# Kernel optimization log

Hardware: AMD Instinct MI355X
Metric: run time of the kernel (lower is better)

Reference implementation:

```python
import jax, jax.numpy as jnp
import numpy as np
import math

H_DIM = 256
EPS = 1e-5


def _bn(x, g, b):
    # BatchNorm1d in training mode: batch stats, biased variance
    mu = x.mean(0)
    var = jnp.var(x, 0)
    return (x - mu) * jax.lax.rsqrt(var + EPS) * g + b


def _batched_corrcoef(x):
    # x: (B, s, n) -> (B, n, n) correlation over n variables with s samples
    xm = x - x.mean(1, keepdims=True)
    c = jnp.einsum('bsi,bsj->bij', xm, xm) / (x.shape[1] - 1)
    d = jnp.sqrt(jnp.diagonal(c, axis1=1, axis2=2))
    c = c / (d[:, :, None] * d[:, None, :])
    return jnp.clip(c, -1.0, 1.0)


def setup_inputs() -> dict:
    key = jax.random.key(0)
    ks = jax.random.split(key, 20)
    h = H_DIM
    s = 0.02
    inp = {
        'x': jax.random.normal(ks[0], (8, 64, 64, h), jnp.float32),
        'e_s': jax.random.normal(ks[1], (8, h), jnp.float32),
        # query/key embeds
        'qW': jax.random.normal(ks[2], (h, h), jnp.float32) * s,
        'qb': jnp.zeros((h,), jnp.float32),
        'kW': jax.random.normal(ks[3], (h, h), jnp.float32) * s,
        'kb': jnp.zeros((h,), jnp.float32),
        # MLP: Linear(h*h, h) + BN + ReLU + Linear(h, h) + BN + ReLU
        'm1W': jax.random.normal(ks[4], (h * h, h), jnp.float32) * s,
        'm1b': jnp.zeros((h,), jnp.float32),
        'm1g': jnp.ones((h,), jnp.float32),
        'm1beta': jnp.zeros((h,), jnp.float32),
        'm2W': jax.random.normal(ks[5], (h, h), jnp.float32) * s,
        'm2b': jnp.zeros((h,), jnp.float32),
        'm2g': jnp.ones((h,), jnp.float32),
        'm2beta': jnp.zeros((h,), jnp.float32),
        # MLP2: Linear(2h, h) + BN + ReLU + Linear(h, h) + BN + ReLU
        'p1W': jax.random.normal(ks[6], (2 * h, h), jnp.float32) * s,
        'p1b': jnp.zeros((h,), jnp.float32),
        'p1g': jnp.ones((h,), jnp.float32),
        'p1beta': jnp.zeros((h,), jnp.float32),
        'p2W': jax.random.normal(ks[7], (h, h), jnp.float32) * s,
        'p2b': jnp.zeros((h,), jnp.float32),
        'p2g': jnp.ones((h,), jnp.float32),
        'p2beta': jnp.zeros((h,), jnp.float32),
    }
    return inp


def reference(x, e_s, qW, qb, kW, kb,
              m1W, m1b, m1g, m1beta, m2W, m2b, m2g, m2beta,
              p1W, p1b, p1g, p1beta, p2W, p2b, p2g, p2beta):
    B, T, S, N = x.shape
    # batched Pearson correlation per (b, t)
    fc = _batched_corrcoef(x.reshape(B * T, S, N))          # (BT, N, N)
    fc = fc.reshape(B * T, N * N)
    h = jax.nn.relu(_bn(fc @ m1W + m1b, m1g, m1beta))
    h = jax.nn.relu(_bn(h @ m2W + m2b, m2g, m2beta))        # (BT, N)
    fc_seq = h.reshape(B, T, N)
    es = jnp.broadcast_to(e_s[:, None, :], (B, T, N))
    Hcat = jnp.concatenate([fc_seq, es], -1).reshape(B * T, 2 * N)
    Hh = jax.nn.relu(_bn(Hcat @ p1W + p1b, p1g, p1beta))
    Hh = jax.nn.relu(_bn(Hh @ p2W + p2b, p2g, p2beta))
    Hh = Hh.reshape(B, T, N)
    # sigmoid query-key attention over time
    x_q = Hh.mean(1, keepdims=True) @ qW + qb               # (B, 1, N)
    x_k = Hh @ kW + kb                                      # (B, T, N)
    att = jax.nn.sigmoid(
        jnp.einsum('bqc,btc->bqt', x_q, x_k) / math.sqrt(x_q.shape[-1])
    )[:, 0]                                                 # (B, T)
    # dropout in eval mode (identity)
    return Hh * att[:, :, None]
```

## Files before the change

### kernel.cpp

```cpp
#include <hip/hip_runtime.h>
#include <stdint.h>
#include <stddef.h>


typedef short short8 __attribute__((ext_vector_type(8)));
typedef float f32x4 __attribute__((ext_vector_type(4)));

#define DEV __device__ __forceinline__

DEV unsigned short f2bf(float f){
  union { float f; unsigned u; } v; v.f = f;
  unsigned r = v.u + 0x7FFFu + ((v.u >> 16) & 1u);
  return (unsigned short)(r >> 16);
}
DEV float bf2f(unsigned short b){
  union { unsigned u; float f; } v; v.u = ((unsigned)b) << 16;
  return v.f;
}
DEV void gload_lds16(const void* g, void* l){
  __builtin_amdgcn_global_load_lds(
      (const __attribute__((address_space(1))) unsigned int*)g,
      (__attribute__((address_space(3))) unsigned int*)l, 16, 0, 0);
}

DEV void tri_decode(int t, int& i, int& jc){
  int a, u;
  if (t < 64)       { a = 0; u = t; }
  else if (t < 192) { a = 1; u = t - 64; }
  else if (t < 384) { a = 2; u = t - 192; }
  else              { a = 3; u = t - 384; }
  int idx = (a == 0) ? u : (a == 1) ? (u >> 1) : (a == 2) ? (u / 3) : (u >> 2);
  jc = u - idx * (a + 1);
  i = 64*a + idx;
}

__global__ __launch_bounds__(256) void k_wtf(const float* __restrict__ W,
                                             unsigned short* __restrict__ WTf,
                                             const float* __restrict__ m2W,
                                             const float* __restrict__ p1W,
                                             const float* __restrict__ p2W,
                                             const float* __restrict__ kW,
                                             unsigned short* __restrict__ WTs,
                                             float2* __restrict__ SQ){
  __shared__ float tile [64][65];
  __shared__ float tile2[64][65];
  const int tr = threadIdx.x >> 6, tc = threadIdx.x & 63;
  const int bid = blockIdx.x;

  if (bid >= 2560){
    const int sub = bid - 2560;
    if (sub == 0){
      for (int i = threadIdx.x; i < 1024; i += 256) SQ[i] = make_float2(0.f, 0.f);
    }
    const int bx = sub >> 2, oy = sub & 3;
    const float* Ws; int K; size_t dst; int kt;
    if (bx < 4)       { Ws = m2W; K = 256; dst = 0;      kt = bx; }
    else if (bx < 12) { Ws = p1W; K = 512; dst = 65536;  kt = bx - 4; }
    else if (bx < 16) { Ws = p2W; K = 256; dst = 196608; kt = bx - 12; }
    else              { Ws = kW;  K = 256; dst = 262144; kt = bx - 16; }
    const int k0 = kt*64, o0 = oy*64;
    #pragma unroll
    for (int q = 0; q < 16; ++q){
      int kr = q*4 + tr;
      tile[kr][tc] = Ws[(size_t)(k0+kr)*256 + o0 + tc];
    }
    __syncthreads();
    #pragma unroll
    for (int q = 0; q < 16; ++q){
      int orow = q*4 + tr;
      WTs[dst + (size_t)(o0+orow)*K + k0 + tc] = f2bf(tile[tc][orow]);
    }
    return;
  }

  int i, jc;
  tri_decode(bid >> 2, i, jc);
  const int j0 = jc * 64;
  const int o0 = (bid & 3) * 64;
  #pragma unroll
  for (int q = 0; q < 16; ++q){
    int kr = q*4 + tr;
    tile [kr][tc] = W[(size_t)(i*256 + j0 + kr)*256 + o0 + tc];
    tile2[kr][tc] = W[(size_t)((j0 + kr)*256 + i)*256 + o0 + tc];
  }
  __syncthreads();
  #pragma unroll
  for (int q = 0; q < 16; ++q){
    int orow = q*4 + tr;
    int j = j0 + tc;
    float v = (j < i) ? (tile[tc][orow] + tile2[tc][orow])
            : (j == i) ? tile[tc][orow] : 0.f;
    WTf[(size_t)(o0+orow)*65536 + (size_t)i*256 + j0 + tc] = f2bf(v);
  }
}

__global__ __launch_bounds__(256) void k_corr2(const float* __restrict__ x,
                                               unsigned short* __restrict__ fc){
  __shared__ unsigned short yT[256*72];
  __shared__ float rs[256];
  __shared__ unsigned short twbuf[4][16*264];
  const int bt = blockIdx.x;
  const float* xb = x + (size_t)bt * 16384;
  const int i = threadIdx.x;

  float sum = 0.f;
  #pragma unroll 8
  for (int s = 0; s < 64; ++s) sum += xb[s*256 + i];
  const float mean = sum * (1.f/64.f);

  float ss = 0.f;
  unsigned int* yT32 = (unsigned int*)yT;
  #pragma unroll 4
  for (int s = 0; s < 64; s += 2){
    float v0 = xb[s*256 + i] - mean;
    float v1 = xb[(s+1)*256 + i] - mean;
    unsigned short b0 = f2bf(v0), b1 = f2bf(v1);
    float r0 = bf2f(b0), r1 = bf2f(b1);
    ss += r0*r0 + r1*r1;
    yT32[(i*72 + s) >> 1] = (unsigned)b0 | ((unsigned)b1 << 16);
  }
  rs[i] = rsqrtf(ss);
  __syncthreads();

  const int w   = threadIdx.x >> 6;
  const int l   = threadIdx.x & 63;
  const int l15 = l & 15, lg = l >> 4;
  const int rtiles[4] = {2*w, 2*w + 1, 14 - 2*w, 15 - 2*w};
  unsigned short* tw = twbuf[w];

  for (int q = 0; q < 4; ++q){
    const int rt = rtiles[q];
    const int band = rt >> 2;
    const int ccmax = 2*band + 1;

    short8 RF[2];
    #pragma unroll
    for (int ks = 0; ks < 2; ++ks)
      RF[ks] = *(const short8*)&yT[(rt*16 + l15)*72 + ks*32 + lg*8];
    float rrow[4];
    #pragma unroll
    for (int r = 0; r < 4; ++r) rrow[r] = rs[rt*16 + lg*4 + r];

    for (int cc = 0; cc <= ccmax; ++cc){
      short8 CF[2][2];
      #pragma unroll
      for (int ct = 0; ct < 2; ++ct){
        int col = cc*32 + ct*16 + l15;
        #pragma unroll
        for (int ks = 0; ks < 2; ++ks)
          CF[ct][ks] = *(const short8*)&yT[col*72 + ks*32 + lg*8];
      }
      f32x4 acc[2];
      #pragma unroll
      for (int ct = 0; ct < 2; ++ct) acc[ct] = (f32x4){0.f,0.f,0.f,0.f};
      #pragma unroll
      for (int ks = 0; ks < 2; ++ks)
        #pragma unroll
        for (int ct = 0; ct < 2; ++ct)
          acc[ct] = __builtin_amdgcn_mfma_f32_16x16x32_bf16(
              RF[ks], CF[ct][ks], acc[ct], 0, 0, 0);
      float rc[2] = { rs[cc*32 + l15], rs[cc*32 + 16 + l15] };
      #pragma unroll
      for (int ct = 0; ct < 2; ++ct)
        #pragma unroll
        for (int r = 0; r < 4; ++r){
          float v = acc[ct][r] * rrow[r] * rc[ct];
          v = fminf(fmaxf(v, -1.f), 1.f);
          tw[(lg*4 + r)*264 + cc*32 + ct*16 + l15] = f2bf(v);
        }
    }
    const int nc  = (ccmax + 1) * 32;
    const int spr = nc >> 3;
    const int total = spr << 4;
    for (int s = l; s < total; s += 64){
      int r  = s / spr;
      int co = (s - r*spr) * 8;
      short8 v = *(const short8*)&tw[r*264 + co];
      *(short8*)&fc[(size_t)bt*65536 + (size_t)(rt*16 + r)*256 + co] = v;
    }
  }
}

__global__ __launch_bounds__(256) void k_gemm(const unsigned short* __restrict__ fc,
                                              const unsigned short* __restrict__ WTf,
                                              float* __restrict__ P){
  __shared__ unsigned short Al[2][64*64];
  __shared__ unsigned short Bl[2][128*64];
  const int bid  = blockIdx.x;
  const int wgid = (bid & 7)*80 + (bid >> 3);
  const int g    = wgid >> 4;
  const int rem  = wgid & 15;
  const int n0   = (rem >> 3) * 128;
  const int m0   = (rem & 7) * 64;
  const int t    = threadIdx.x;
  const int w = t >> 6, l = t & 63, l15 = l & 15, lg = l >> 4;
  const int wr = (w >> 1) * 32;
  const int wc = (w & 1) * 64;

  auto stage = [&](int bsel, int s2){
    int ti, tjc;
    tri_decode(g*16 + s2, ti, tjc);
    const int kk = ti*256 + tjc*64;
    #pragma unroll
    for (int i2 = 0; i2 < 2; ++i2){
      int c = i2*256 + t;
      int row = c >> 3, ch = c & 7;
      int sch = ch ^ (row & 7);
      gload_lds16(fc + (size_t)(m0+row)*65536 + kk + sch*8, &Al[bsel][c*8]);
    }
    #pragma unroll
    for (int i2 = 0; i2 < 4; ++i2){
      int c = i2*256 + t;
      int row = c >> 3, ch = c & 7;
      int sch = ch ^ (row & 7);
      gload_lds16(WTf + (size_t)(n0+row)*65536 + kk + sch*8, &Bl[bsel][c*8]);
    }
  };

  f32x4 acc[2][4];
  #pragma unroll
  for (int a = 0; a < 2; ++a)
    #pragma unroll
    for (int b = 0; b < 4; ++b) acc[a][b] = (f32x4){0.f,0.f,0.f,0.f};

  stage(0, 0);
  int cur = 0;
  for (int s2 = 0; s2 < 16; ++s2){
    __syncthreads();
    if (s2 < 15) stage(cur ^ 1, s2 + 1);
    #pragma unroll
    for (int ks = 0; ks < 2; ++ks){
      short8 af[2], bf[4];
      #pragma unroll
      for (int rt = 0; rt < 2; ++rt){
        int row = wr + rt*16 + l15;
        int pch = (ks*4 + lg) ^ (row & 7);
        af[rt] = *(const short8*)&Al[cur][row*64 + pch*8];
      }
      #pragma unroll
      for (int ct = 0; ct < 4; ++ct){
        int row = wc + ct*16 + l15;
        int pch = (ks*4 + lg) ^ (row & 7);
        bf[ct] = *(const short8*)&Bl[cur][row*64 + pch*8];
      }
      #pragma unroll
      for (int rt = 0; rt < 2; ++rt)
        #pragma unroll
        for (int ct = 0; ct < 4; ++ct)
          acc[rt][ct] = __builtin_amdgcn_mfma_f32_16x16x32_bf16(
              af[rt], bf[ct], acc[rt][ct], 0, 0, 0);
    }
    cur ^= 1;
  }

  float* Pb = P + (size_t)g * 131072;
  #pragma unroll
  for (int rt = 0; rt < 2; ++rt)
    #pragma unroll
    for (int ct = 0; ct < 4; ++ct)
      #pragma unroll
      for (int r = 0; r < 4; ++r){
        int row = m0 + wr + rt*16 + lg*4 + r;
        int col = n0 + wc + ct*16 + l15;
        Pb[(size_t)row*256 + col] = acc[rt][ct][r];
      }
}

__global__ __launch_bounds__(256) void k_reduce(const float* __restrict__ P,
                                                float* __restrict__ z,
                                                float2* __restrict__ SQ1){
  __shared__ float4 ex[128];
  const int t = threadIdx.x;
  const int row = blockIdx.x*2 + (t >> 7);
  const int c2  = (t & 127) * 2;
  float sx = 0.f, sy = 0.f;
  #pragma unroll 8
  for (int ks = 0; ks < 40; ++ks){
    const float* p = &P[(size_t)ks*131072 + row*256 + c2];
    sx += p[0]; sy += p[1];
  }
  z[row*256 + c2]     = sx;
  z[row*256 + c2 + 1] = sy;
  if (t >= 128) ex[t & 127] = make_float4(sx, sx*sx, sy, sy*sy);
  __syncthreads();
  if (t < 128){
    float4 o = ex[t];
    atomicAdd(&SQ1[c2].x,     sx + o.x);
    atomicAdd(&SQ1[c2].y,     sx*sx + o.y);
    atomicAdd(&SQ1[c2 + 1].x, sy + o.z);
    atomicAdd(&SQ1[c2 + 1].y, sy*sy + o.w);
  }
}

template<int KK, int NC64, bool CAT>
__global__ __launch_bounds__(256) void k_sgm(const float* __restrict__ zin,
                                             const float* __restrict__ es,
                                             const unsigned short* __restrict__ WTl_g,
                                             const float2* __restrict__ SQin,
                                             const float* __restrict__ g,
                                             const float* __restrict__ be,
                                             float2* __restrict__ SQout,
                                             float* __restrict__ zout){
  constexpr int NCOLS = NC64 * 64;
  constexpr int NP = KK / 64;
  __shared__ unsigned short Bl[NP][NCOLS*64];
  __shared__ float2 ssl[256];
  const int r0 = blockIdx.x * 16;
  const int n0 = blockIdx.y * NCOLS;
  const int b  = r0 >> 6;
  const int t = threadIdx.x;
  const int l = t & 63, l15 = l & 15, lg = (l >> 4) & 3;
  const int w = t >> 6;
  const int wc = w * (NCOLS/4);

  #pragma unroll
  for (int p = 0; p < NP; ++p){
    #pragma unroll
    for (int i = 0; i < NCOLS*8/256; ++i){
      int c = i*256 + t;
      int row = c >> 3, ch = c & 7;
      int sch = ch ^ (row & 7);
      gload_lds16(WTl_g + (size_t)(n0+row)*KK + p*64 + sch*8, &Bl[p][c*8]);
    }
  }
  {
    float2 sq = SQin[t];
    float mu  = sq.x * (1.f/512.f);
    float var = sq.y * (1.f/512.f) - mu*mu;
    float sc  = g[t] * rsqrtf(var + 1e-5f);
    ssl[t] = make_float2(sc, be[t] - mu*sc);
  }
  __syncthreads();

  short8 a[KK/32];
  #pragma unroll
  for (int ks = 0; ks < KK/32; ++ks){
    int k = ks*32 + lg*8;
    short8 v;
    if (!CAT || k < 256){
      f32x4 lo = *(const f32x4*)&zin[(size_t)(r0+l15)*256 + k];
      f32x4 hi = *(const f32x4*)&zin[(size_t)(r0+l15)*256 + k + 4];
      #pragma unroll
      for (int j = 0; j < 4; ++j){
        float2 sv0 = ssl[k+j];
        float2 sv1 = ssl[k+4+j];
        v[j]   = (short)f2bf(fmaxf(lo[j]*sv0.x + sv0.y, 0.f));
        v[4+j] = (short)f2bf(fmaxf(hi[j]*sv1.x + sv1.y, 0.f));
      }
    } else {
      f32x4 lo = *(const f32x4*)&es[b*256 + (k-256)];
      f32x4 hi = *(const f32x4*)&es[b*256 + (k-256) + 4];
      #pragma unroll
      for (int j = 0; j < 4; ++j){
        v[j]   = (short)f2bf(lo[j]);
        v[4+j] = (short)f2bf(hi[j]);
      }
    }
    a[ks] = v;
  }

  f32x4 acc[NC64];
  #pragma unroll
  for (int ct = 0; ct < NC64; ++ct) acc[ct] = (f32x4){0.f,0.f,0.f,0.f};
  #pragma unroll
  for (int ks = 0; ks < KK/32; ++ks){
    int p = ks >> 1;
    int kin = (ks & 1) * 4;
    #pragma unroll
    for (int ct = 0; ct < NC64; ++ct){
      int row = wc + ct*16 + l15;
      int pch = (kin + lg) ^ (row & 7);
      short8 bfr = *(const short8*)&Bl[p][row*64 + pch*8];
      acc[ct] = __builtin_amdgcn_mfma_f32_16x16x32_bf16(a[ks], bfr, acc[ct], 0, 0, 0);
    }
  }

  #pragma unroll
  for (int ct = 0; ct < NC64; ++ct){
    int col = n0 + wc + ct*16 + l15;
    #pragma unroll
    for (int r = 0; r < 4; ++r)
      zout[(size_t)(r0 + lg*4 + r)*256 + col] = acc[ct][r];
    float S = acc[ct][0] + acc[ct][1] + acc[ct][2] + acc[ct][3];
    float Q = acc[ct][0]*acc[ct][0] + acc[ct][1]*acc[ct][1]
            + acc[ct][2]*acc[ct][2] + acc[ct][3]*acc[ct][3];
    S += __shfl_xor(S, 16); S += __shfl_xor(S, 32);
    Q += __shfl_xor(Q, 16); Q += __shfl_xor(Q, 32);
    if ((l >> 4) == 0){
      atomicAdd(&SQout[col].x, S);
      atomicAdd(&SQout[col].y, Q);
    }
  }
}

__global__ __launch_bounds__(256) void k_qmean2(const float* __restrict__ z4,
                                                const float2* __restrict__ SQ4,
                                                const float* __restrict__ g,
                                                const float* __restrict__ be,
                                                const float* __restrict__ qW,
                                                const float* __restrict__ qb,
                                                float* __restrict__ q){
  __shared__ float qWl[256*64];
  __shared__ float hm[256];
  __shared__ float part[4][64];
  const int b  = blockIdx.x & 7;
  const int n0 = (blockIdx.x >> 3) * 64;
  const int t  = threadIdx.x;

  #pragma unroll
  for (int it = 0; it < 16; ++it){
    int s4 = it*256 + t;
    int k  = s4 >> 4;
    int c  = (s4 & 15) * 4;
    gload_lds16(qW + (size_t)k*256 + n0 + c, (char*)qWl + (size_t)s4*16);
  }
  {
    float2 sq = SQ4[t];
    float mu  = sq.x * (1.f/512.f);
    float var = sq.y * (1.f/512.f) - mu*mu;
    float sc  = g[t] * rsqrtf(var + 1e-5f);
    float sh  = be[t] - mu*sc;
    float s = 0.f;
    #pragma unroll 8
    for (int tt = 0; tt < 64; ++tt)
      s += fmaxf(z4[(size_t)((b<<6)+tt)*256 + t]*sc + sh, 0.f);
    hm[t] = s * (1.f/64.f);
  }
  __syncthreads();

  const int col = t & 63, kq = t >> 6;
  float a = 0.f;
  #pragma unroll 8
  for (int k2 = 0; k2 < 64; ++k2){
    int k = kq*64 + k2;
    a += hm[k] * qWl[k*64 + col];
  }
  part[kq][col] = a;
  __syncthreads();
  if (t < 64)
    q[b*256 + n0 + t] = part[0][t] + part[1][t] + part[2][t] + part[3][t] + qb[n0 + t];
}

__global__ __launch_bounds__(256) void k_att2(const float* __restrict__ z4,
                                              const float2* __restrict__ SQ4,
                                              const float* __restrict__ g,
                                              const float* __restrict__ be,
                                              const unsigned short* __restrict__ kWT,
                                              const float* __restrict__ kb,
                                              const float* __restrict__ qv,
                                              float* __restrict__ out){
  __shared__ unsigned short Bl[4][256*64];
  __shared__ float2 ssl[256];
  __shared__ float Hh[16][260];
  __shared__ float pr[4][16];
  __shared__ float sig[16];
  const int r0 = blockIdx.x * 16;
  const int b  = r0 >> 6;
  const int t = threadIdx.x;
  const int l = t & 63, l15 = l & 15, lg = (l >> 4) & 3;
  const int w = t >> 6;
  const int wc = w * 64;

  #pragma unroll
  for (int p = 0; p < 4; ++p){
    #pragma unroll
    for (int i = 0; i < 8; ++i){
      int c = i*256 + t;
      int row = c >> 3, ch = c & 7;
      int sch = ch ^ (row & 7);
      gload_lds16(kWT + (size_t)row*256 + p*64 + sch*8, &Bl[p][c*8]);
    }
  }
  {
    float2 sq = SQ4[t];
    float mu  = sq.x * (1.f/512.f);
    float var = sq.y * (1.f/512.f) - mu*mu;
    float sc  = g[t] * rsqrtf(var + 1e-5f);
    ssl[t] = make_float2(sc, be[t] - mu*sc);
  }
  __syncthreads();

  short8 a[8];
  #pragma unroll
  for (int ks = 0; ks < 8; ++ks){
    int k = ks*32 + lg*8;
    f32x4 lo = *(const f32x4*)&z4[(size_t)(r0+l15)*256 + k];
    f32x4 hi = *(const f32x4*)&z4[(size_t)(r0+l15)*256 + k + 4];
    short8 v;
    f32x4 h0, h1;
    #pragma unroll
    for (int j = 0; j < 4; ++j){
      float2 sv0 = ssl[k+j];
      float2 sv1 = ssl[k+4+j];
      float x0 = fmaxf(lo[j]*sv0.x + sv0.y, 0.f);
      float x1 = fmaxf(hi[j]*sv1.x + sv1.y, 0.f);
      h0[j] = x0; h1[j] = x1;
      v[j]   = (short)f2bf(x0);
      v[4+j] = (short)f2bf(x1);
    }
    a[ks] = v;
    *(f32x4*)&Hh[l15][k]     = h0;
    *(f32x4*)&Hh[l15][k + 4] = h1;
  }

  f32x4 acc[4];
  #pragma unroll
  for (int ct = 0; ct < 4; ++ct) acc[ct] = (f32x4){0.f,0.f,0.f,0.f};
  #pragma unroll
  for (int ks = 0; ks < 8; ++ks){
    int p = ks >> 1;
    int kin = (ks & 1) * 4;
    #pragma unroll
    for (int ct = 0; ct < 4; ++ct){
      int row = wc + ct*16 + l15;
      int pch = (kin + lg) ^ (row & 7);
      short8 bfr = *(const short8*)&Bl[p][row*64 + pch*8];
      acc[ct] = __builtin_amdgcn_mfma_f32_16x16x32_bf16(a[ks], bfr, acc[ct], 0, 0, 0);
    }
  }

  float p4[4] = {0.f, 0.f, 0.f, 0.f};
  #pragma unroll
  for (int ct = 0; ct < 4; ++ct){
    int col = wc + ct*16 + l15;
    float qc  = qv[b*256 + col];
    float kbc = kb[col];
    #pragma unroll
    for (int r = 0; r < 4; ++r) p4[r] += (acc[ct][r] + kbc) * qc;
  }
  #pragma unroll
  for (int r = 0; r < 4; ++r){
    p4[r] += __shfl_xor(p4[r], 1);
    p4[r] += __shfl_xor(p4[r], 2);
    p4[r] += __shfl_xor(p4[r], 4);
    p4[r] += __shfl_xor(p4[r], 8);
  }
  if (l15 == 0){
    #pragma unroll
    for (int r = 0; r < 4; ++r) pr[w][lg*4 + r] = p4[r];
  }
  __syncthreads();
  if (t < 16){
    float s = pr[0][t] + pr[1][t] + pr[2][t] + pr[3][t];
    sig[t] = 1.f / (1.f + __expf(-s * (1.f/16.f)));
  }
  __syncthreads();
  #pragma unroll
  for (int r = 0; r < 16; ++r)
    out[(size_t)(r0+r)*256 + t] = Hh[r][t] * sig[r];
}

extern "C" void kernel_launch(void* const* d_in, const int* in_sizes, int n_in,
                              void* d_out, int out_size, void* d_ws, size_t ws_size,
                              hipStream_t stream){
  (void)in_sizes; (void)n_in; (void)out_size; (void)ws_size;
  const float* x    = (const float*)d_in[0];
  const float* e_s  = (const float*)d_in[1];
  const float* qW   = (const float*)d_in[2];
  const float* qb   = (const float*)d_in[3];
  const float* kW   = (const float*)d_in[4];
  const float* kb   = (const float*)d_in[5];
  const float* m1W  = (const float*)d_in[6];
  const float* m1g  = (const float*)d_in[8];
  const float* m1be = (const float*)d_in[9];
  const float* m2W  = (const float*)d_in[10];
  const float* m2g  = (const float*)d_in[12];
  const float* m2be = (const float*)d_in[13];
  const float* p1W  = (const float*)d_in[14];
  const float* p1g  = (const float*)d_in[16];
  const float* p1be = (const float*)d_in[17];
  const float* p2W  = (const float*)d_in[18];
  const float* p2g  = (const float*)d_in[20];
  const float* p2be = (const float*)d_in[21];

  char* ws = (char*)d_ws;
  unsigned short* WTf = (unsigned short*)ws; ws += 33554432;
  unsigned short* fc  = (unsigned short*)ws; ws += 67108864;
  float* P            = (float*)ws;  ws += 33554432;
  float* z1           = (float*)ws;  ws += 524288;
  float* z2           = (float*)ws;  ws += 524288;
  float* z3           = (float*)ws;  ws += 524288;
  float* z4           = (float*)ws;  ws += 524288;
  unsigned short* WTs = (unsigned short*)ws; ws += 655360;
  float2* SQ          = (float2*)ws; ws += 8192;
  float* qvv          = (float*)ws;  ws += 8192;
  float* out = (float*)d_out;

  const unsigned short* m2WT = WTs;
  const unsigned short* p1WT = WTs + 65536;
  const unsigned short* p2WT = WTs + 196608;
  const unsigned short* kWT  = WTs + 262144;
  float2* SQ1 = SQ, *SQ2 = SQ + 256, *SQ3 = SQ + 512, *SQ4 = SQ + 768;

  k_wtf   <<<2640, 256, 0, stream>>>(m1W, WTf, m2W, p1W, p2W, kW, WTs, SQ);
  k_corr2 <<<512, 256, 0, stream>>>(x, fc);
  k_gemm  <<<640, 256, 0, stream>>>(fc, WTf, P);
  k_reduce<<<256, 256, 0, stream>>>(P, z1, SQ1);
  k_sgm<256,1,false><<<dim3(32,4), 256, 0, stream>>>(z1, nullptr, m2WT, SQ1, m1g, m1be, SQ2, z2);
  k_sgm<512,1,true> <<<dim3(32,4), 256, 0, stream>>>(z2, e_s, p1WT, SQ2, m2g, m2be, SQ3, z3);
  k_sgm<256,1,false><<<dim3(32,4), 256, 0, stream>>>(z3, nullptr, p2WT, SQ3, p1g, p1be, SQ4, z4);
  k_qmean2<<<32, 256, 0, stream>>>(z4, SQ4, p2g, p2be, qW, qb, qvv);
  k_att2  <<<32, 256, 0, stream>>>(z4, SQ4, p2g, p2be, kWT, kb, qvv, out);
}
```

Baseline: 121.0 us.

## Fuse split-K reduction into GEMM via last-block-done atomic counter

Removes the separate k_reduce launch. Each GEMM tile increments a per-output-tile counter, and the 40th arriving block sums the 40 split-K partials for its 64x128 tile. It then writes z1 and accumulates the BN column sums and squared sums through LDS and global atomics. This saves a kernel launch and lets the reduction overlap with still-running GEMM blocks, at the cost of threadfences and a serialized tail reduction done by only 16 blocks.

```diff
diff --git a/kernel.cpp b/kernel.cpp
--- a/kernel.cpp
+++ b/kernel.cpp
@@ -41,7 +41,8 @@
                                              const float* __restrict__ p2W,
                                              const float* __restrict__ kW,
                                              unsigned short* __restrict__ WTs,
-                                             float2* __restrict__ SQ){
+                                             float2* __restrict__ SQ,
+                                             unsigned* __restrict__ cnt){
   __shared__ float tile [64][65];
   __shared__ float tile2[64][65];
   const int tr = threadIdx.x >> 6, tc = threadIdx.x & 63;
@@ -51,6 +52,7 @@
     const int sub = bid - 2560;
     if (sub == 0){
       for (int i = threadIdx.x; i < 1024; i += 256) SQ[i] = make_float2(0.f, 0.f);
+      if (threadIdx.x < 16) cnt[threadIdx.x] = 0u;
     }
     const int bx = sub >> 2, oy = sub & 3;
     const float* Ws; int K; size_t dst; int kt;
@@ -183,9 +185,14 @@
 
 __global__ __launch_bounds__(256) void k_gemm(const unsigned short* __restrict__ fc,
                                               const unsigned short* __restrict__ WTf,
-                                              float* __restrict__ P){
+                                              float* __restrict__ P,
+                                              float* __restrict__ z1,
+                                              float2* __restrict__ SQ1,
+                                              unsigned* __restrict__ cnt){
   __shared__ unsigned short Al[2][64*64];
   __shared__ unsigned short Bl[2][128*64];
+  __shared__ unsigned doneS;
+  __shared__ float2 sqs[128];
   const int bid  = blockIdx.x;
   const int wgid = (bid & 7)*80 + (bid >> 3);
   const int g    = wgid >> 4;
@@ -264,31 +271,55 @@
         int col = n0 + wc + ct*16 + l15;
         Pb[(size_t)row*256 + col] = acc[rt][ct][r];
       }
-}
-
-__global__ __launch_bounds__(256) void k_reduce(const float* __restrict__ P,
-                                                float* __restrict__ z,
-                                                float2* __restrict__ SQ1){
-  __shared__ float4 ex[128];
-  const int t = threadIdx.x;
-  const int row = blockIdx.x*2 + (t >> 7);
-  const int c2  = (t & 127) * 2;
-  float sx = 0.f, sy = 0.f;
-  #pragma unroll 8
-  for (int ks = 0; ks < 40; ++ks){
-    const float* p = &P[(size_t)ks*131072 + row*256 + c2];
-    sx += p[0]; sy += p[1];
-  }
-  z[row*256 + c2]     = sx;
-  z[row*256 + c2 + 1] = sy;
-  if (t >= 128) ex[t & 127] = make_float4(sx, sx*sx, sy, sy*sy);
+
+  __threadfence();
+  __syncthreads();
+  if (t == 0) doneS = atomicAdd(&cnt[rem], 1u);
+  __syncthreads();
+  if (doneS != 39u) return;
+  __threadfence();
+  if (t < 128) sqs[t] = make_float2(0.f, 0.f);
+
+  const int fr = t >> 2;
+  const int cb = (t & 3) * 32;
+  f32x4 accf[8];
+  #pragma unroll
+  for (int j = 0; j < 8; ++j) accf[j] = (f32x4){0.f,0.f,0.f,0.f};
+  for (int g2 = 0; g2 < 40; ++g2){
+    const float* ps = P + (size_t)g2*131072 + (size_t)(m0+fr)*256 + n0 + cb;
+    #pragma unroll
+    for (int j = 0; j < 8; ++j) accf[j] += *(const f32x4*)&ps[j*4];
+  }
+  #pragma unroll
+  for (int j = 0; j < 8; ++j)
+    *(f32x4*)&z1[(size_t)(m0+fr)*256 + n0 + cb + j*4] = accf[j];
+
+  f32x4 qf[8];
+  #pragma unroll
+  for (int j = 0; j < 8; ++j) qf[j] = accf[j]*accf[j];
+  #pragma unroll
+  for (int st = 4; st < 64; st <<= 1)
+    #pragma unroll
+    for (int j = 0; j < 8; ++j)
+      #pragma unroll
+      for (int e = 0; e < 4; ++e){
+        accf[j][e] += __shfl_xor(accf[j][e], st);
+        qf[j][e]   += __shfl_xor(qf[j][e],  st);
+      }
+  __syncthreads();
+  if (l < 4){
+    #pragma unroll
+    for (int j = 0; j < 8; ++j)
+      #pragma unroll
+      for (int e = 0; e < 4; ++e){
+        atomicAdd(&sqs[cb + j*4 + e].x, accf[j][e]);
+        atomicAdd(&sqs[cb + j*4 + e].y, qf[j][e]);
+      }
+  }
   __syncthreads();
   if (t < 128){
-    float4 o = ex[t];
-    atomicAdd(&SQ1[c2].x,     sx + o.x);
-    atomicAdd(&SQ1[c2].y,     sx*sx + o.y);
-    atomicAdd(&SQ1[c2 + 1].x, sy + o.z);
-    atomicAdd(&SQ1[c2 + 1].y, sy*sy + o.w);
+    atomicAdd(&SQ1[n0 + t].x, sqs[t].x);
+    atomicAdd(&SQ1[n0 + t].y, sqs[t].y);
   }
 }
 
@@ -583,6 +614,7 @@
   float* z4           = (float*)ws;  ws += 524288;
   unsigned short* WTs = (unsigned short*)ws; ws += 655360;
   float2* SQ          = (float2*)ws; ws += 8192;
+  unsigned* cnt       = (unsigned*)ws; ws += 64;
   float* qvv          = (float*)ws;  ws += 8192;
   float* out = (float*)d_out;
 
@@ -592,10 +624,9 @@
   const unsigned short* kWT  = WTs + 262144;
   float2* SQ1 = SQ, *SQ2 = SQ + 256, *SQ3 = SQ + 512, *SQ4 = SQ + 768;
 
-  k_wtf   <<<2640, 256, 0, stream>>>(m1W, WTf, m2W, p1W, p2W, kW, WTs, SQ);
+  k_wtf   <<<2640, 256, 0, stream>>>(m1W, WTf, m2W, p1W, p2W, kW, WTs, SQ, cnt);
   k_corr2 <<<512, 256, 0, stream>>>(x, fc);
-  k_gemm  <<<640, 256, 0, stream>>>(fc, WTf, P);
-  k_reduce<<<256, 256, 0, stream>>>(P, z1, SQ1);
+  k_gemm  <<<640, 256, 0, stream>>>(fc, WTf, P, z1, SQ1, cnt);
   k_sgm<256,1,false><<<dim3(32,4), 256, 0, stream>>>(z1, nullptr, m2WT, SQ1, m1g, m1be, SQ2, z2);
   k_sgm<512,1,true> <<<dim3(32,4), 256, 0, stream>>>(z2, e_s, p1WT, SQ2, m2g, m2be, SQ3, z3);
   k_sgm<256,1,false><<<dim3(32,4), 256, 0, stream>>>(z3, nullptr, p2WT, SQ3, p1g, p1be, SQ4, z4);
```

After: 216.8 us. +79.2%, slower.
